# Optimization experiments

Measured on AMD Instinct MI355X. Metric: run time of the kernel, lower is better.

Reference implementation:

```python
import jax, jax.numpy as jnp
import numpy as np
from jax import lax

EPS_GN = 1e-5
EPS_LN = 1e-5
EPS_ADJ = 1e-6


def group_norm(x, g, b, groups=8, eps=EPS_GN):
    # x: (N, C, T); PyTorch GroupNorm: normalize over (C//groups, T) per group
    N, C, T = x.shape
    xr = x.reshape(N, groups, C // groups, T)
    m = xr.mean(axis=(2, 3), keepdims=True)
    v = xr.var(axis=(2, 3), keepdims=True)
    xr = (xr - m) * lax.rsqrt(v + eps)
    return xr.reshape(N, C, T) * g[None, :, None] + b[None, :, None]


def layer_norm(x, g, b, eps=EPS_LN):
    m = x.mean(axis=-1, keepdims=True)
    v = x.var(axis=-1, keepdims=True)
    return (x - m) * lax.rsqrt(v + eps) * g + b


def conv1d(x, w, stride, pad):
    # x: (N, Cin, T), w: (Cout, Cin, K), no bias
    return lax.conv_general_dilated(x, w, window_strides=(stride,), padding=[(pad, pad)],
                                    dimension_numbers=('NCH', 'OIH', 'NCH'))


def setup_inputs() -> dict:
    key = jax.random.key(0)
    ks = jax.random.split(key, 16)
    B, C, T = 256, 4, 4096
    TW, D, N = 64, 128, 4
    x = jax.random.normal(ks[0], (B, C, T), dtype=jnp.float32)
    conv1_w = jax.random.normal(ks[1], (TW, 1, 9), dtype=jnp.float32) * 0.1
    gn1_g = jnp.ones((TW,), jnp.float32)
    gn1_b = jnp.zeros((TW,), jnp.float32)
    conv2_w = jax.random.normal(ks[2], (TW, TW, 7), dtype=jnp.float32) * 0.05
    gn2_g = jnp.ones((TW,), jnp.float32)
    gn2_b = jnp.zeros((TW,), jnp.float32)
    proj_w = jax.random.normal(ks[3], (D, TW), dtype=jnp.float32) * 0.1
    proj_b = jnp.zeros((D,), jnp.float32)
    A = jnp.eye(N, dtype=jnp.float32) + 0.05 * jax.random.normal(ks[4], (N, N), dtype=jnp.float32)
    lin1_w = jax.random.normal(ks[5], (D, D), dtype=jnp.float32) * 0.08
    ln1_g = jnp.ones((D,), jnp.float32)
    ln1_b = jnp.zeros((D,), jnp.float32)
    lin2_w = jax.random.normal(ks[6], (D, D), dtype=jnp.float32) * 0.08
    ln2_g = jnp.ones((D,), jnp.float32)
    ln2_b = jnp.zeros((D,), jnp.float32)
    on_g = jnp.ones((D,), jnp.float32)
    on_b = jnp.zeros((D,), jnp.float32)
    return dict(x=x, conv1_w=conv1_w, gn1_g=gn1_g, gn1_b=gn1_b, conv2_w=conv2_w,
                gn2_g=gn2_g, gn2_b=gn2_b, proj_w=proj_w, proj_b=proj_b, A=A,
                lin1_w=lin1_w, ln1_g=ln1_g, ln1_b=ln1_b, lin2_w=lin2_w,
                ln2_g=ln2_g, ln2_b=ln2_b, on_g=on_g, on_b=on_b)


def reference(x, conv1_w, gn1_g, gn1_b, conv2_w, gn2_g, gn2_b, proj_w, proj_b, A,
              lin1_w, ln1_g, ln1_b, lin2_w, ln2_g, ln2_b, on_g, on_b):
    B, C, T = x.shape
    D = proj_w.shape[0]
    # The per-channel Python loop in the original shares the same temporal net;
    # fold channels into the batch dim and run the convs once.
    h = x.reshape(B * C, 1, T)
    h = jax.nn.gelu(group_norm(conv1d(h, conv1_w, 2, 4), gn1_g, gn1_b), approximate=False)
    h = jax.nn.gelu(group_norm(conv1d(h, conv2_w, 2, 3), gn2_g, gn2_b), approximate=False)
    h = h.mean(axis=-1)                      # (B*C, TW)
    v = h @ proj_w.T + proj_b                # (B*C, D)
    H = v.reshape(B, C, D)                   # node features, N = C channels
    # normalized adjacency: D^{-1/2} (A + I) D^{-1/2}
    A_tilde = A + jnp.eye(A.shape[0], dtype=A.dtype)
    deg = A_tilde.sum(axis=1)
    d_inv_sqrt = (deg + EPS_ADJ) ** -0.5
    A_hat = d_inv_sqrt[:, None] * A_tilde * d_inv_sqrt[None, :]
    for lw, lg, lb in ((lin1_w, ln1_g, ln1_b), (lin2_w, ln2_g, ln2_b)):
        Hm = jnp.einsum('nm,bmd->bnd', A_hat, H)
        H = jax.nn.gelu(layer_norm(Hm @ lw.T, lg, lb), approximate=False)
    H = layer_norm(H, on_g, on_b)
    return H.mean(axis=1)                    # (B, D)
```

## Files before the change

### kernel.cpp

```cpp
#include <hip/hip_runtime.h>
#include <hip/hip_fp16.h>
#include <math.h>

#define NS   1024
#define TIN  4096
#define T1   2048
#define T2   1024
#define TW   64
#define NG   8
#define DD   128

typedef __attribute__((ext_vector_type(8))) _Float16 f16x8;
typedef __attribute__((ext_vector_type(4))) float    f32x4;

__device__ __forceinline__ float gelu_fast(float x) {
  float t = x * x;
  float p = fmaf(0.044715f, t, 1.0f);
  float u = 2.3022038f * x * p;
  float e = exp2f(u);
  float r = __builtin_amdgcn_rcpf(e + 1.0f);
  return fmaf(-x, r, x);
}

__global__ __launch_bounds__(64) void k_stats1(
    const float* __restrict__ x, const float* __restrict__ w1,
    float* __restrict__ stats1) {
  int n = blockIdx.x;
  __shared__ float xw[4112];
  const float* xr = x + (size_t)n * TIN;
  for (int i = threadIdx.x; i < 4112; i += 64) {
    int xi = i - 4;
    xw[i] = (xi >= 0 && xi < TIN) ? xr[xi] : 0.f;
  }
  __syncthreads();
  float C[45], S[9];
#pragma unroll
  for (int c = 0; c < 45; c++) C[c] = 0.f;
#pragma unroll
  for (int i = 0; i < 9; i++) S[i] = 0.f;
  int l = threadIdx.x;
  for (int j = 0; j < 32; j++) {
    int t = l + 64 * j;
    float w[9];
#pragma unroll
    for (int i = 0; i < 9; i++) w[i] = xw[2 * t + i];
#pragma unroll
    for (int i = 0; i < 9; i++) S[i] += w[i];
    int c = 0;
#pragma unroll
    for (int i = 0; i < 9; i++)
#pragma unroll
      for (int jj = i; jj < 9; jj++) { C[c] = fmaf(w[i], w[jj], C[c]); c++; }
  }
#pragma unroll
  for (int off = 1; off < 64; off <<= 1) {
#pragma unroll
    for (int i = 0; i < 9; i++) S[i] += __shfl_xor(S[i], off, 64);
#pragma unroll
    for (int c = 0; c < 45; c++) C[c] += __shfl_xor(C[c], off, 64);
  }
  float wv[9];
#pragma unroll
  for (int i = 0; i < 9; i++) wv[i] = w1[l * 9 + i];
  float sm = 0.f, sq = 0.f;
  {
    int c = 0;
#pragma unroll
    for (int i = 0; i < 9; i++) {
      sm = fmaf(wv[i], S[i], sm);
#pragma unroll
      for (int jj = i; jj < 9; jj++) {
        float f = (jj == i) ? wv[i] * wv[jj] : 2.f * wv[i] * wv[jj];
        sq = fmaf(f, C[c], sq); c++;
      }
    }
  }
#pragma unroll
  for (int off = 1; off < 8; off <<= 1) {
    sm += __shfl_xor(sm, off, 64);
    sq += __shfl_xor(sq, off, 64);
  }
  if ((l & 7) == 0) {
    float m = sm * (1.f / 16384.f);
    float v = sq * (1.f / 16384.f) - m * m;
    stats1[(n * NG + (l >> 3)) * 2 + 0] = m;
    stats1[(n * NG + (l >> 3)) * 2 + 1] = rsqrtf(v + 1e-5f);
  }
}

__global__ __launch_bounds__(256) void k_prep(
    const float* __restrict__ w2, const float* __restrict__ w1,
    _Float16* __restrict__ w2tf, _Float16* __restrict__ w1h) {
  int idx = blockIdx.x * 256 + threadIdx.x;
  if (idx < 7 * 64 * 64) {
    int kk = idx >> 12;
    int r = idx & 4095;
    int co = r >> 6, ci = r & 63;
    w2tf[idx] = (_Float16)w2[(co * 64 + ci) * 7 + kk];
  } else {
    int r = idx - 28672;
    if (r < 64 * 32) {
      int ci = r >> 5, k = r & 31;
      w1h[r] = (k < 9) ? (_Float16)w1[ci * 9 + k] : (_Float16)0.f;
    }
  }
}

__global__ __launch_bounds__(256, 6) void k_conv(
    const float* __restrict__ x, const _Float16* __restrict__ w1h,
    const float* __restrict__ g1, const float* __restrict__ b1,
    const float* __restrict__ stats1, const _Float16* __restrict__ w2tf,
    __half* __restrict__ y2, float* __restrict__ stats2) {
  constexpr int ROWS = 144, HS = 72;
  __shared__ _Float16 h1s[ROWS * HS];
  __shared__ _Float16 xh[320];
  __shared__ float scs[TW], bss[TW];

  const int tid = threadIdx.x;
  const int n = blockIdx.x >> 4;
  const int tile = blockIdx.x & 15;
  const int t0 = tile << 6;
  const bool chk = (tile == 0) || (tile == 15);

  const float* xr = x + (size_t)n * TIN;
  for (int i = tid; i < 320; i += 256) {
    int xi = 4 * t0 - 10 + i;
    xh[i] = (i < 278 && xi >= 0 && xi < TIN) ? (_Float16)xr[xi] : (_Float16)0.f;
  }
  if (tid < TW) {
    int ci = tid, g = ci >> 3;
    float m = stats1[(n * NG + g) * 2 + 0];
    float is = stats1[(n * NG + g) * 2 + 1];
    float s = is * g1[ci];
    scs[ci] = s;
    bss[ci] = b1[ci] - m * s;
  }
  __syncthreads();

  const int lane = tid & 63;
  const int wv = tid >> 6;
  const int m = lane & 15;
  const int q = lane >> 4;

  {
    f16x8 w1f[4];
#pragma unroll
    for (int nt = 0; nt < 4; nt++)
      w1f[nt] = *(const f16x8*)&w1h[(nt * 16 + m) * 32 + 8 * q];
    float sc4[4], bs4[4];
#pragma unroll
    for (int nt = 0; nt < 4; nt++) {
      sc4[nt] = scs[nt * 16 + m];
      bs4[nt] = bss[nt * 16 + m];
    }
    for (int mt = wv; mt < 9; mt += 4) {
      int r0 = mt * 16;
      int xi0 = 2 * (r0 + m) + 8 * q;
      uint4 uu;
      uu.x = *(const unsigned*)&xh[xi0 + 0];
      uu.y = *(const unsigned*)&xh[xi0 + 2];
      uu.z = *(const unsigned*)&xh[xi0 + 4];
      uu.w = *(const unsigned*)&xh[xi0 + 6];
      f16x8 af = __builtin_bit_cast(f16x8, uu);
      int rowb = r0 + 4 * q;
#pragma unroll
      for (int nt = 0; nt < 4; nt++) {
        f32x4 d = __builtin_amdgcn_mfma_f32_16x16x32_f16(
            af, w1f[nt], (f32x4){0.f, 0.f, 0.f, 0.f}, 0, 0, 0);
#pragma unroll
        for (int r = 0; r < 4; r++) {
          float v = gelu_fast(fmaf(d[r], sc4[nt], bs4[nt]));
          if (chk) {
            int tp = 2 * t0 - 3 + rowb + r;
            if ((unsigned)tp >= (unsigned)T1) v = 0.f;
          }
          h1s[(rowb + r) * HS + nt * 16 + m] = (_Float16)v;
        }
      }
    }
  }
  __syncthreads();

  const int co0 = wv * 16 + m;
  f32x4 acc[4];
#pragma unroll
  for (int mt = 0; mt < 4; mt++) acc[mt] = (f32x4){0.f, 0.f, 0.f, 0.f};

  for (int kk = 0; kk < 7; kk++) {
    f16x8 bfr[2];
#pragma unroll
    for (int ks = 0; ks < 2; ks++)
      bfr[ks] = *(const f16x8*)&w2tf[(kk * 64 + co0) * 64 + 32 * ks + 8 * q];
#pragma unroll
    for (int mt = 0; mt < 4; mt++) {
      int tl = 2 * (mt * 16 + m) + kk;
      f16x8 a0 = *(const f16x8*)&h1s[tl * HS + 8 * q];
      f16x8 a1 = *(const f16x8*)&h1s[tl * HS + 32 + 8 * q];
      acc[mt] = __builtin_amdgcn_mfma_f32_16x16x32_f16(a0, bfr[0], acc[mt], 0, 0, 0);
      acc[mt] = __builtin_amdgcn_mfma_f32_16x16x32_f16(a1, bfr[1], acc[mt], 0, 0, 0);
    }
  }

  float sum = 0.f, ssq = 0.f;
#pragma unroll
  for (int mt = 0; mt < 4; mt++)
#pragma unroll
    for (int r = 0; r < 4; r++) {
      float v = acc[mt][r];
      sum += v; ssq += v * v;
    }
  sum += __shfl_xor(sum, 1, 64);  ssq += __shfl_xor(ssq, 1, 64);
  sum += __shfl_xor(sum, 2, 64);  ssq += __shfl_xor(ssq, 2, 64);
  sum += __shfl_xor(sum, 4, 64);  ssq += __shfl_xor(ssq, 4, 64);
  sum += __shfl_xor(sum, 16, 64); ssq += __shfl_xor(ssq, 16, 64);
  sum += __shfl_xor(sum, 32, 64); ssq += __shfl_xor(ssq, 32, 64);
  if (lane == 0 || lane == 8) {
    int g = 2 * wv + (lane >> 3);
    atomicAdd(&stats2[(n * NG + g) * 2 + 0], sum);
    atomicAdd(&stats2[(n * NG + g) * 2 + 1], ssq);
  }

  __syncthreads();
  __half* tr = (__half*)h1s;
#pragma unroll
  for (int mt = 0; mt < 4; mt++)
#pragma unroll
    for (int r = 0; r < 4; r++) {
      int t = mt * 16 + q * 4 + r;
      tr[t * HS + co0] = __float2half(acc[mt][r]);
    }
  __syncthreads();
  for (int idx = tid; idx < 512; idx += 256) {
    int t = idx >> 3, c8 = (idx & 7) * 8;
    float4 v = *(float4*)&tr[t * HS + c8];
    *(float4*)&y2[((size_t)(n * 1024) + t0 + t) * 64 + c8] = v;
  }
}

__global__ __launch_bounds__(256) void k_gn2mean(
    const __half* __restrict__ y2, const float* __restrict__ stats2,
    const float* __restrict__ g2, const float* __restrict__ b2,
    float* __restrict__ hbar) {
  int n = blockIdx.x;
  int coct = threadIdx.x & 7;
  int tsl = threadIdx.x >> 3;
  int co0 = coct * 8;
  float mn = stats2[(n * NG + coct) * 2 + 0] * (1.f / 8192.f);
  float e2 = stats2[(n * NG + coct) * 2 + 1] * (1.f / 8192.f);
  float istd = rsqrtf(e2 - mn * mn + 1e-5f);
  float sca[8], sh[8];
#pragma unroll
  for (int j = 0; j < 8; j++) {
    sca[j] = istd * g2[co0 + j];
    sh[j] = b2[co0 + j] - mn * sca[j];
  }
  const __half* base = y2 + (size_t)n * 65536;
  float a[8];
#pragma unroll
  for (int j = 0; j < 8; j++) a[j] = 0.f;
  for (int i = 0; i < 32; i++) {
    int t = tsl + 32 * i;
    float4 raw = *(const float4*)&base[t * 64 + co0];
    __half2 hh[4];
    *(float4*)hh = raw;
#pragma unroll
    for (int p = 0; p < 4; p++) {
      float2 f = __half22float2(hh[p]);
      a[2 * p]     += gelu_fast(fmaf(f.x, sca[2 * p], sh[2 * p]));
      a[2 * p + 1] += gelu_fast(fmaf(f.y, sca[2 * p + 1], sh[2 * p + 1]));
    }
  }
  __shared__ float red[32][64];
  *(float4*)&red[tsl][co0] = *(float4*)&a[0];
  *(float4*)&red[tsl][co0 + 4] = *(float4*)&a[4];
  __syncthreads();
  if (threadIdx.x < 64) {
    float s = 0.f;
#pragma unroll 8
    for (int r = 0; r < 32; r++) s += red[r][threadIdx.x];
    hbar[n * 64 + threadIdx.x] = s;
  }
}

__global__ __launch_bounds__(256) void k_head(
    const float* __restrict__ hbar,
    const float* __restrict__ pw, const float* __restrict__ pb,
    const float* __restrict__ A,
    const float* __restrict__ l1w, const float* __restrict__ l1g, const float* __restrict__ l1b,
    const float* __restrict__ l2w, const float* __restrict__ l2g, const float* __restrict__ l2b,
    const float* __restrict__ og, const float* __restrict__ ob,
    float* __restrict__ out) {
  int b = blockIdx.x;
  __shared__ float h4[4][TW];
  __shared__ float H[4][DD];
  __shared__ float Hm[4][DD];
  __shared__ float Xs[4][DD];
  __shared__ float At[16], Ah[16], dinv[4];
  {
    int i = threadIdx.x;
    int c = i >> 6, k = i & 63;
    h4[c][k] = hbar[(b * 4 + c) * TW + k] * (1.f / 1024.f);
  }
  if (threadIdx.x < 16)
    At[threadIdx.x] = A[threadIdx.x] + ((threadIdx.x % 5) == 0 ? 1.f : 0.f);
  __syncthreads();
  if (threadIdx.x < 4) {
    float dg = At[threadIdx.x * 4] + At[threadIdx.x * 4 + 1] +
               At[threadIdx.x * 4 + 2] + At[threadIdx.x * 4 + 3];
    dinv[threadIdx.x] = rsqrtf(dg + 1e-6f);
  }
  for (int idx = threadIdx.x; idx < 512; idx += 256) {
    int c = idx >> 7, d = idx & 127;
    float acc = pb[d];
    const float* wrow = pw + d * TW;
#pragma unroll 8
    for (int k = 0; k < TW; k++) acc += h4[c][k] * wrow[k];
    H[c][d] = acc;
  }
  __syncthreads();
  if (threadIdx.x < 16)
    Ah[threadIdx.x] = dinv[threadIdx.x >> 2] * At[threadIdx.x] * dinv[threadIdx.x & 3];
  __syncthreads();
  for (int L = 0; L < 2; L++) {
    const float* lw = L ? l2w : l1w;
    const float* lg = L ? l2g : l1g;
    const float* lb = L ? l2b : l1b;
    for (int idx = threadIdx.x; idx < 512; idx += 256) {
      int nn = idx >> 7, d = idx & 127;
      Hm[nn][d] = Ah[nn * 4 + 0] * H[0][d] + Ah[nn * 4 + 1] * H[1][d] +
                  Ah[nn * 4 + 2] * H[2][d] + Ah[nn * 4 + 3] * H[3][d];
    }
    __syncthreads();
    for (int idx = threadIdx.x; idx < 512; idx += 256) {
      int nn = idx >> 7, d = idx & 127;
      float acc = 0.f;
      const float* wrow = lw + d * DD;
#pragma unroll 8
      for (int k = 0; k < DD; k++) acc += Hm[nn][k] * wrow[k];
      Xs[nn][d] = acc;
    }
    __syncthreads();
    {
      int w = threadIdx.x >> 6, lane = threadIdx.x & 63;
      float v0 = Xs[w][lane], v1 = Xs[w][lane + 64];
      float s = v0 + v1, qq = v0 * v0 + v1 * v1;
#pragma unroll
      for (int off = 1; off < 64; off <<= 1) {
        s += __shfl_xor(s, off, 64);
        qq += __shfl_xor(qq, off, 64);
      }
      float mm = s * (1.f / 128.f);
      float istd = rsqrtf(qq * (1.f / 128.f) - mm * mm + 1e-5f);
      H[w][lane]      = gelu_fast((v0 - mm) * istd * lg[lane] + lb[lane]);
      H[w][lane + 64] = gelu_fast((v1 - mm) * istd * lg[lane + 64] + lb[lane + 64]);
    }
    __syncthreads();
  }
  {
    int w = threadIdx.x >> 6, lane = threadIdx.x & 63;
    float v0 = H[w][lane], v1 = H[w][lane + 64];
    float s = v0 + v1, qq = v0 * v0 + v1 * v1;
#pragma unroll
    for (int off = 1; off < 64; off <<= 1) {
      s += __shfl_xor(s, off, 64);
      qq += __shfl_xor(qq, off, 64);
    }
    float mm = s * (1.f / 128.f);
    float istd = rsqrtf(qq * (1.f / 128.f) - mm * mm + 1e-5f);
    Xs[w][lane]      = (v0 - mm) * istd * og[lane] + ob[lane];
    Xs[w][lane + 64] = (v1 - mm) * istd * og[lane + 64] + ob[lane + 64];
  }
  __syncthreads();
  if (threadIdx.x < DD) {
    int d = threadIdx.x;
    out[b * DD + d] = 0.25f * (Xs[0][d] + Xs[1][d] + Xs[2][d] + Xs[3][d]);
  }
}

extern "C" void kernel_launch(void* const* d_in, const int* in_sizes, int n_in,
                              void* d_out, int out_size, void* d_ws, size_t ws_size,
                              hipStream_t stream) {
  (void)in_sizes; (void)n_in; (void)out_size; (void)ws_size;
  const float* x       = (const float*)d_in[0];
  const float* conv1_w = (const float*)d_in[1];
  const float* gn1_g   = (const float*)d_in[2];
  const float* gn1_b   = (const float*)d_in[3];
  const float* conv2_w = (const float*)d_in[4];
  const float* gn2_g   = (const float*)d_in[5];
  const float* gn2_b   = (const float*)d_in[6];
  const float* proj_w  = (const float*)d_in[7];
  const float* proj_b  = (const float*)d_in[8];
  const float* A       = (const float*)d_in[9];
  const float* lin1_w  = (const float*)d_in[10];
  const float* ln1_g   = (const float*)d_in[11];
  const float* ln1_b   = (const float*)d_in[12];
  const float* lin2_w  = (const float*)d_in[13];
  const float* ln2_g   = (const float*)d_in[14];
  const float* ln2_b   = (const float*)d_in[15];
  const float* on_g    = (const float*)d_in[16];
  const float* on_b    = (const float*)d_in[17];
  float* out = (float*)d_out;

  float* wsf = (float*)d_ws;
  float* stats2 = wsf;
  float* stats1 = wsf + 16384;
  float* hbar   = wsf + 32768;
  _Float16* w2tf = (_Float16*)(wsf + 98304);
  _Float16* w1h  = (_Float16*)(wsf + 112640);
  __half* y2h    = (__half*)(wsf + 113664);

  hipMemsetAsync(stats2, 0, 16384 * sizeof(float), stream);
  k_prep<<<120, 256, 0, stream>>>(conv2_w, conv1_w, w2tf, w1h);
  k_stats1<<<NS, 64, 0, stream>>>(x, conv1_w, stats1);
  k_conv<<<NS * 16, 256, 0, stream>>>(x, w1h, gn1_g, gn1_b, stats1, w2tf,
                                      y2h, stats2);
  k_gn2mean<<<NS, 256, 0, stream>>>(y2h, stats2, gn2_g, gn2_b, hbar);
  k_head<<<256, 256, 0, stream>>>(hbar, proj_w, proj_b, A,
                                  lin1_w, ln1_g, ln1_b,
                                  lin2_w, ln2_g, ln2_b,
                                  on_g, on_b, out);
}
```

Measured before the change: 331.8 us.

## Fuse conv2, GN2 stats and GELU-mean into one per-sample block kernel

Replaces the tiled conv kernel plus separate GN2+mean kernel with a single 1024-thread block per sample that computes all 16 time tiles in four passes. Conv2 outputs stay in registers as packed fp16, group statistics are reduced in shared memory, and GELU+mean is applied directly. This removes the y2 global round-trip, the stats2 atomics and memset, and one launch. In exchange it needs 32 held registers per thread, a large LDS footprint (about 92KB), fewer blocks (1024), and more block-wide barriers, all of which may limit occupancy.

```diff
diff --git a/kernel.cpp b/kernel.cpp
--- a/kernel.cpp
+++ b/kernel.cpp
@@ -106,61 +106,72 @@
   }
 }
 
-__global__ __launch_bounds__(256, 6) void k_conv(
+__global__ __launch_bounds__(1024, 4) void k_fused(
     const float* __restrict__ x, const _Float16* __restrict__ w1h,
     const float* __restrict__ g1, const float* __restrict__ b1,
     const float* __restrict__ stats1, const _Float16* __restrict__ w2tf,
-    __half* __restrict__ y2, float* __restrict__ stats2) {
-  constexpr int ROWS = 144, HS = 72;
-  __shared__ _Float16 h1s[ROWS * HS];
-  __shared__ _Float16 xh[320];
+    const float* __restrict__ g2, const float* __restrict__ b2,
+    float* __restrict__ hbar) {
+  constexpr int HS = 72;
+  __shared__ _Float16 xh[4160];
+  __shared__ _Float16 h1s[4][144 * HS];
   __shared__ float scs[TW], bss[TW];
+  __shared__ float redS[256], redQ[256];
+  __shared__ float scb[TW], shb[TW];
 
   const int tid = threadIdx.x;
-  const int n = blockIdx.x >> 4;
-  const int tile = blockIdx.x & 15;
-  const int t0 = tile << 6;
-  const bool chk = (tile == 0) || (tile == 15);
-
+  const int n = blockIdx.x;
   const float* xr = x + (size_t)n * TIN;
-  for (int i = tid; i < 320; i += 256) {
-    int xi = 4 * t0 - 10 + i;
-    xh[i] = (i < 278 && xi >= 0 && xi < TIN) ? (_Float16)xr[xi] : (_Float16)0.f;
+  for (int i = tid; i < 4160; i += 1024) {
+    int xi = i - 10;
+    xh[i] = (xi >= 0 && xi < TIN) ? (_Float16)xr[xi] : (_Float16)0.f;
   }
   if (tid < TW) {
     int ci = tid, g = ci >> 3;
-    float m = stats1[(n * NG + g) * 2 + 0];
+    float mn = stats1[(n * NG + g) * 2 + 0];
     float is = stats1[(n * NG + g) * 2 + 1];
     float s = is * g1[ci];
     scs[ci] = s;
-    bss[ci] = b1[ci] - m * s;
-  }
-  __syncthreads();
-
+    bss[ci] = b1[ci] - mn * s;
+  }
+  __syncthreads();
+
+  const int w = tid >> 6;
   const int lane = tid & 63;
-  const int wv = tid >> 6;
   const int m = lane & 15;
   const int q = lane >> 4;
-
-  {
-    f16x8 w1f[4];
-#pragma unroll
-    for (int nt = 0; nt < 4; nt++)
-      w1f[nt] = *(const f16x8*)&w1h[(nt * 16 + m) * 32 + 8 * q];
-    float sc4[4], bs4[4];
-#pragma unroll
-    for (int nt = 0; nt < 4; nt++) {
-      sc4[nt] = scs[nt * 16 + m];
-      bs4[nt] = bss[nt * 16 + m];
-    }
-    for (int mt = wv; mt < 9; mt += 4) {
+  const int ti = w >> 2;
+  const int wvt = w & 3;
+  const int co0 = wvt * 16 + m;
+
+  f16x8 w1f[4];
+#pragma unroll
+  for (int nt = 0; nt < 4; nt++)
+    w1f[nt] = *(const f16x8*)&w1h[(nt * 16 + m) * 32 + 8 * q];
+  float sc4[4], bs4[4];
+#pragma unroll
+  for (int nt = 0; nt < 4; nt++) {
+    sc4[nt] = scs[nt * 16 + m];
+    bs4[nt] = bss[nt * 16 + m];
+  }
+
+  unsigned held[32];
+  float ssum = 0.f, ssq = 0.f;
+
+  for (int it = 0; it < 4; it++) {
+    const int tg = it * 4 + ti;
+    const int t0 = tg << 6;
+    const bool chk = (tg == 0) || (tg == 15);
+    __syncthreads();
+
+    for (int mt = wvt; mt < 9; mt += 4) {
       int r0 = mt * 16;
-      int xi0 = 2 * (r0 + m) + 8 * q;
+      int xg = 4 * t0 + 2 * (r0 + m) + 8 * q;
       uint4 uu;
-      uu.x = *(const unsigned*)&xh[xi0 + 0];
-      uu.y = *(const unsigned*)&xh[xi0 + 2];
-      uu.z = *(const unsigned*)&xh[xi0 + 4];
-      uu.w = *(const unsigned*)&xh[xi0 + 6];
+      uu.x = *(const unsigned*)&xh[xg + 0];
+      uu.y = *(const unsigned*)&xh[xg + 2];
+      uu.z = *(const unsigned*)&xh[xg + 4];
+      uu.w = *(const unsigned*)&xh[xg + 6];
       f16x8 af = __builtin_bit_cast(f16x8, uu);
       int rowb = r0 + 4 * q;
 #pragma unroll
@@ -174,111 +185,80 @@
             int tp = 2 * t0 - 3 + rowb + r;
             if ((unsigned)tp >= (unsigned)T1) v = 0.f;
           }
-          h1s[(rowb + r) * HS + nt * 16 + m] = (_Float16)v;
+          h1s[ti][(rowb + r) * HS + nt * 16 + m] = (_Float16)v;
         }
       }
     }
-  }
-  __syncthreads();
-
-  const int co0 = wv * 16 + m;
-  f32x4 acc[4];
-#pragma unroll
-  for (int mt = 0; mt < 4; mt++) acc[mt] = (f32x4){0.f, 0.f, 0.f, 0.f};
-
-  for (int kk = 0; kk < 7; kk++) {
-    f16x8 bfr[2];
-#pragma unroll
-    for (int ks = 0; ks < 2; ks++)
-      bfr[ks] = *(const f16x8*)&w2tf[(kk * 64 + co0) * 64 + 32 * ks + 8 * q];
-#pragma unroll
-    for (int mt = 0; mt < 4; mt++) {
-      int tl = 2 * (mt * 16 + m) + kk;
-      f16x8 a0 = *(const f16x8*)&h1s[tl * HS + 8 * q];
-      f16x8 a1 = *(const f16x8*)&h1s[tl * HS + 32 + 8 * q];
-      acc[mt] = __builtin_amdgcn_mfma_f32_16x16x32_f16(a0, bfr[0], acc[mt], 0, 0, 0);
-      acc[mt] = __builtin_amdgcn_mfma_f32_16x16x32_f16(a1, bfr[1], acc[mt], 0, 0, 0);
-    }
-  }
-
-  float sum = 0.f, ssq = 0.f;
-#pragma unroll
-  for (int mt = 0; mt < 4; mt++)
-#pragma unroll
-    for (int r = 0; r < 4; r++) {
-      float v = acc[mt][r];
-      sum += v; ssq += v * v;
-    }
-  sum += __shfl_xor(sum, 1, 64);  ssq += __shfl_xor(ssq, 1, 64);
-  sum += __shfl_xor(sum, 2, 64);  ssq += __shfl_xor(ssq, 2, 64);
-  sum += __shfl_xor(sum, 4, 64);  ssq += __shfl_xor(ssq, 4, 64);
-  sum += __shfl_xor(sum, 16, 64); ssq += __shfl_xor(ssq, 16, 64);
-  sum += __shfl_xor(sum, 32, 64); ssq += __shfl_xor(ssq, 32, 64);
-  if (lane == 0 || lane == 8) {
-    int g = 2 * wv + (lane >> 3);
-    atomicAdd(&stats2[(n * NG + g) * 2 + 0], sum);
-    atomicAdd(&stats2[(n * NG + g) * 2 + 1], ssq);
-  }
-
-  __syncthreads();
-  __half* tr = (__half*)h1s;
-#pragma unroll
-  for (int mt = 0; mt < 4; mt++)
-#pragma unroll
-    for (int r = 0; r < 4; r++) {
-      int t = mt * 16 + q * 4 + r;
-      tr[t * HS + co0] = __float2half(acc[mt][r]);
-    }
-  __syncthreads();
-  for (int idx = tid; idx < 512; idx += 256) {
-    int t = idx >> 3, c8 = (idx & 7) * 8;
-    float4 v = *(float4*)&tr[t * HS + c8];
-    *(float4*)&y2[((size_t)(n * 1024) + t0 + t) * 64 + c8] = v;
-  }
-}
-
-__global__ __launch_bounds__(256) void k_gn2mean(
-    const __half* __restrict__ y2, const float* __restrict__ stats2,
-    const float* __restrict__ g2, const float* __restrict__ b2,
-    float* __restrict__ hbar) {
-  int n = blockIdx.x;
-  int coct = threadIdx.x & 7;
-  int tsl = threadIdx.x >> 3;
-  int co0 = coct * 8;
-  float mn = stats2[(n * NG + coct) * 2 + 0] * (1.f / 8192.f);
-  float e2 = stats2[(n * NG + coct) * 2 + 1] * (1.f / 8192.f);
-  float istd = rsqrtf(e2 - mn * mn + 1e-5f);
-  float sca[8], sh[8];
-#pragma unroll
-  for (int j = 0; j < 8; j++) {
-    sca[j] = istd * g2[co0 + j];
-    sh[j] = b2[co0 + j] - mn * sca[j];
-  }
-  const __half* base = y2 + (size_t)n * 65536;
-  float a[8];
-#pragma unroll
-  for (int j = 0; j < 8; j++) a[j] = 0.f;
+    __syncthreads();
+
+    f32x4 acc[4];
+#pragma unroll
+    for (int mt = 0; mt < 4; mt++) acc[mt] = (f32x4){0.f, 0.f, 0.f, 0.f};
+    for (int kk = 0; kk < 7; kk++) {
+      f16x8 bf0 = *(const f16x8*)&w2tf[(kk * 64 + co0) * 64 + 8 * q];
+      f16x8 bf1 = *(const f16x8*)&w2tf[(kk * 64 + co0) * 64 + 32 + 8 * q];
+#pragma unroll
+      for (int mt = 0; mt < 4; mt++) {
+        int tl = 2 * (mt * 16 + m) + kk;
+        f16x8 a0 = *(const f16x8*)&h1s[ti][tl * HS + 8 * q];
+        f16x8 a1 = *(const f16x8*)&h1s[ti][tl * HS + 32 + 8 * q];
+        acc[mt] = __builtin_amdgcn_mfma_f32_16x16x32_f16(a0, bf0, acc[mt], 0, 0, 0);
+        acc[mt] = __builtin_amdgcn_mfma_f32_16x16x32_f16(a1, bf1, acc[mt], 0, 0, 0);
+      }
+    }
+
+#pragma unroll
+    for (int mt = 0; mt < 4; mt++)
+#pragma unroll
+      for (int pr = 0; pr < 2; pr++) {
+        float lo = acc[mt][2 * pr], hi = acc[mt][2 * pr + 1];
+        ssum += lo + hi;
+        ssq += lo * lo + hi * hi;
+        held[it * 8 + mt * 2 + pr] =
+            __builtin_bit_cast(unsigned, __builtin_amdgcn_cvt_pkrtz(lo, hi));
+      }
+  }
+
+  ssum += __shfl_xor(ssum, 16, 64); ssq += __shfl_xor(ssq, 16, 64);
+  ssum += __shfl_xor(ssum, 32, 64); ssq += __shfl_xor(ssq, 32, 64);
+  if (q == 0) { redS[w * 16 + m] = ssum; redQ[w * 16 + m] = ssq; }
+  __syncthreads();
+  if (tid < 64) {
+    int wt = tid >> 4, mm = tid & 15;
+    float s  = redS[wt * 16 + mm] + redS[(wt + 4) * 16 + mm] +
+               redS[(wt + 8) * 16 + mm] + redS[(wt + 12) * 16 + mm];
+    float q2 = redQ[wt * 16 + mm] + redQ[(wt + 4) * 16 + mm] +
+               redQ[(wt + 8) * 16 + mm] + redQ[(wt + 12) * 16 + mm];
+    s  += __shfl_xor(s, 1, 64);  q2 += __shfl_xor(q2, 1, 64);
+    s  += __shfl_xor(s, 2, 64);  q2 += __shfl_xor(q2, 2, 64);
+    s  += __shfl_xor(s, 4, 64);  q2 += __shfl_xor(q2, 4, 64);
+    float mn = s * (1.f / 8192.f);
+    float e2 = q2 * (1.f / 8192.f);
+    float istd = rsqrtf(e2 - mn * mn + 1e-5f);
+    float sca = istd * g2[tid];
+    scb[tid] = sca;
+    shb[tid] = b2[tid] - mn * sca;
+  }
+  __syncthreads();
+
+  float sca = scb[co0], sh = shb[co0];
+  float tsum = 0.f;
+#pragma unroll
   for (int i = 0; i < 32; i++) {
-    int t = tsl + 32 * i;
-    float4 raw = *(const float4*)&base[t * 64 + co0];
-    __half2 hh[4];
-    *(float4*)hh = raw;
-#pragma unroll
-    for (int p = 0; p < 4; p++) {
-      float2 f = __half22float2(hh[p]);
-      a[2 * p]     += gelu_fast(fmaf(f.x, sca[2 * p], sh[2 * p]));
-      a[2 * p + 1] += gelu_fast(fmaf(f.y, sca[2 * p + 1], sh[2 * p + 1]));
-    }
-  }
-  __shared__ float red[32][64];
-  *(float4*)&red[tsl][co0] = *(float4*)&a[0];
-  *(float4*)&red[tsl][co0 + 4] = *(float4*)&a[4];
-  __syncthreads();
-  if (threadIdx.x < 64) {
-    float s = 0.f;
-#pragma unroll 8
-    for (int r = 0; r < 32; r++) s += red[r][threadIdx.x];
-    hbar[n * 64 + threadIdx.x] = s;
+    __half2 hh = __builtin_bit_cast(__half2, held[i]);
+    float2 f = __half22float2(hh);
+    tsum += gelu_fast(fmaf(f.x, sca, sh)) + gelu_fast(fmaf(f.y, sca, sh));
+  }
+  tsum += __shfl_xor(tsum, 16, 64);
+  tsum += __shfl_xor(tsum, 32, 64);
+  __syncthreads();
+  if (q == 0) redS[w * 16 + m] = tsum;
+  __syncthreads();
+  if (tid < 64) {
+    int wt = tid >> 4, mm = tid & 15;
+    float s = redS[wt * 16 + mm] + redS[(wt + 4) * 16 + mm] +
+              redS[(wt + 8) * 16 + mm] + redS[(wt + 12) * 16 + mm];
+    hbar[n * TW + tid] = s;
   }
 }
 
@@ -402,19 +382,15 @@
   float* out = (float*)d_out;
 
   float* wsf = (float*)d_ws;
-  float* stats2 = wsf;
-  float* stats1 = wsf + 16384;
-  float* hbar   = wsf + 32768;
-  _Float16* w2tf = (_Float16*)(wsf + 98304);
-  _Float16* w1h  = (_Float16*)(wsf + 112640);
-  __half* y2h    = (__half*)(wsf + 113664);
-
-  hipMemsetAsync(stats2, 0, 16384 * sizeof(float), stream);
+  float* stats1 = wsf;
+  float* hbar   = wsf + 16384;
+  _Float16* w2tf = (_Float16*)(wsf + 81920);
+  _Float16* w1h  = w2tf + 28672;
+
   k_prep<<<120, 256, 0, stream>>>(conv2_w, conv1_w, w2tf, w1h);
   k_stats1<<<NS, 64, 0, stream>>>(x, conv1_w, stats1);
-  k_conv<<<NS * 16, 256, 0, stream>>>(x, w1h, gn1_g, gn1_b, stats1, w2tf,
-                                      y2h, stats2);
-  k_gn2mean<<<NS, 256, 0, stream>>>(y2h, stats2, gn2_g, gn2_b, hbar);
+  k_fused<<<NS, 1024, 0, stream>>>(x, w1h, gn1_g, gn1_b, stats1, w2tf,
+                                   gn2_g, gn2_b, hbar);
   k_head<<<256, 256, 0, stream>>>(hbar, proj_w, proj_b, A,
                                   lin1_w, ln1_g, ln1_b,
                                   lin2_w, ln2_g, ln2_b,
```

Result: slower. 416.1 us (+25.4%).

## Transpose conv1 MFMA output, pad LDS rows, and reorder conv2 weights per output channel

Applied to the files above, without the earlier changes.

The conv1 MFMA operands are swapped so each lane holds four consecutive channels of one row. The four GELU outputs are then packed to fp16 and written to LDS as a single 8-byte store, replacing four scalar stores, and the boundary mask is evaluated once per row. The LDS row stride changes from 72 to 76 halves to alter the bank pattern. The conv2 weights are re-laid out as [co][kk][ci] and the kk loop is fully unrolled with precomputed pointers. Occupancy bounds drop from 6 to 4 blocks per CU, and the fp16 conversion switches to round-toward-zero.

```diff
diff --git a/kernel.cpp b/kernel.cpp
--- a/kernel.cpp
+++ b/kernel.cpp
@@ -93,9 +93,9 @@
     _Float16* __restrict__ w2tf, _Float16* __restrict__ w1h) {
   int idx = blockIdx.x * 256 + threadIdx.x;
   if (idx < 7 * 64 * 64) {
-    int kk = idx >> 12;
-    int r = idx & 4095;
-    int co = r >> 6, ci = r & 63;
+    int co = idx / 448;
+    int r = idx % 448;
+    int kk = r >> 6, ci = r & 63;
     w2tf[idx] = (_Float16)w2[(co * 64 + ci) * 7 + kk];
   } else {
     int r = idx - 28672;
@@ -106,15 +106,15 @@
   }
 }
 
-__global__ __launch_bounds__(256, 6) void k_conv(
+#define HS 76
+__global__ __launch_bounds__(256, 4) void k_conv(
     const float* __restrict__ x, const _Float16* __restrict__ w1h,
     const float* __restrict__ g1, const float* __restrict__ b1,
     const float* __restrict__ stats1, const _Float16* __restrict__ w2tf,
     __half* __restrict__ y2, float* __restrict__ stats2) {
-  constexpr int ROWS = 144, HS = 72;
-  __shared__ _Float16 h1s[ROWS * HS];
+  __shared__ _Float16 h1s[144 * HS];
   __shared__ _Float16 xh[320];
-  __shared__ float scs[TW], bss[TW];
+  __shared__ __align__(16) float scs[TW], bss[TW];
 
   const int tid = threadIdx.x;
   const int n = blockIdx.x >> 4;
@@ -147,35 +147,39 @@
 #pragma unroll
     for (int nt = 0; nt < 4; nt++)
       w1f[nt] = *(const f16x8*)&w1h[(nt * 16 + m) * 32 + 8 * q];
-    float sc4[4], bs4[4];
+    float4 scv[4], bsv[4];
 #pragma unroll
     for (int nt = 0; nt < 4; nt++) {
-      sc4[nt] = scs[nt * 16 + m];
-      bs4[nt] = bss[nt * 16 + m];
+      scv[nt] = *(const float4*)&scs[nt * 16 + 4 * q];
+      bsv[nt] = *(const float4*)&bss[nt * 16 + 4 * q];
     }
     for (int mt = wv; mt < 9; mt += 4) {
-      int r0 = mt * 16;
-      int xi0 = 2 * (r0 + m) + 8 * q;
+      int row = mt * 16 + m;
+      int xg = 2 * row + 8 * q;
       uint4 uu;
-      uu.x = *(const unsigned*)&xh[xi0 + 0];
-      uu.y = *(const unsigned*)&xh[xi0 + 2];
-      uu.z = *(const unsigned*)&xh[xi0 + 4];
-      uu.w = *(const unsigned*)&xh[xi0 + 6];
-      f16x8 af = __builtin_bit_cast(f16x8, uu);
-      int rowb = r0 + 4 * q;
+      uu.x = *(const unsigned*)&xh[xg + 0];
+      uu.y = *(const unsigned*)&xh[xg + 2];
+      uu.z = *(const unsigned*)&xh[xg + 4];
+      uu.w = *(const unsigned*)&xh[xg + 6];
+      f16x8 bf = __builtin_bit_cast(f16x8, uu);
+      bool oor = false;
+      if (chk) {
+        int tp = 2 * t0 - 3 + row;
+        oor = ((unsigned)tp >= (unsigned)T1);
+      }
 #pragma unroll
       for (int nt = 0; nt < 4; nt++) {
         f32x4 d = __builtin_amdgcn_mfma_f32_16x16x32_f16(
-            af, w1f[nt], (f32x4){0.f, 0.f, 0.f, 0.f}, 0, 0, 0);
-#pragma unroll
-        for (int r = 0; r < 4; r++) {
-          float v = gelu_fast(fmaf(d[r], sc4[nt], bs4[nt]));
-          if (chk) {
-            int tp = 2 * t0 - 3 + rowb + r;
-            if ((unsigned)tp >= (unsigned)T1) v = 0.f;
-          }
-          h1s[(rowb + r) * HS + nt * 16 + m] = (_Float16)v;
-        }
+            w1f[nt], bf, (f32x4){0.f, 0.f, 0.f, 0.f}, 0, 0, 0);
+        float v0 = gelu_fast(fmaf(d[0], scv[nt].x, bsv[nt].x));
+        float v1 = gelu_fast(fmaf(d[1], scv[nt].y, bsv[nt].y));
+        float v2 = gelu_fast(fmaf(d[2], scv[nt].z, bsv[nt].z));
+        float v3 = gelu_fast(fmaf(d[3], scv[nt].w, bsv[nt].w));
+        uint2 pk;
+        pk.x = __builtin_bit_cast(unsigned, __builtin_amdgcn_cvt_pkrtz(v0, v1));
+        pk.y = __builtin_bit_cast(unsigned, __builtin_amdgcn_cvt_pkrtz(v2, v3));
+        if (oor) { pk.x = 0u; pk.y = 0u; }
+        *(uint2*)&h1s[row * HS + nt * 16 + 4 * q] = pk;
       }
     }
   }
@@ -186,19 +190,33 @@
 #pragma unroll
   for (int mt = 0; mt < 4; mt++) acc[mt] = (f32x4){0.f, 0.f, 0.f, 0.f};
 
+  const _Float16* wp = w2tf + co0 * 448 + 8 * q;
+  const _Float16* ap0 = &h1s[(2 * (0 * 16 + m)) * HS + 8 * q];
+  const _Float16* ap1 = &h1s[(2 * (1 * 16 + m)) * HS + 8 * q];
+  const _Float16* ap2 = &h1s[(2 * (2 * 16 + m)) * HS + 8 * q];
+  const _Float16* ap3 = &h1s[(3 * 16 + m) * 2 * HS + 8 * q];
+
+#pragma unroll
   for (int kk = 0; kk < 7; kk++) {
-    f16x8 bfr[2];
-#pragma unroll
-    for (int ks = 0; ks < 2; ks++)
-      bfr[ks] = *(const f16x8*)&w2tf[(kk * 64 + co0) * 64 + 32 * ks + 8 * q];
-#pragma unroll
-    for (int mt = 0; mt < 4; mt++) {
-      int tl = 2 * (mt * 16 + m) + kk;
-      f16x8 a0 = *(const f16x8*)&h1s[tl * HS + 8 * q];
-      f16x8 a1 = *(const f16x8*)&h1s[tl * HS + 32 + 8 * q];
-      acc[mt] = __builtin_amdgcn_mfma_f32_16x16x32_f16(a0, bfr[0], acc[mt], 0, 0, 0);
-      acc[mt] = __builtin_amdgcn_mfma_f32_16x16x32_f16(a1, bfr[1], acc[mt], 0, 0, 0);
-    }
+    f16x8 b0 = *(const f16x8*)(wp + kk * 64);
+    f16x8 b1 = *(const f16x8*)(wp + kk * 64 + 32);
+    f16x8 a;
+    a = *(const f16x8*)(ap0 + kk * HS);
+    acc[0] = __builtin_amdgcn_mfma_f32_16x16x32_f16(a, b0, acc[0], 0, 0, 0);
+    a = *(const f16x8*)(ap0 + kk * HS + 32);
+    acc[0] = __builtin_amdgcn_mfma_f32_16x16x32_f16(a, b1, acc[0], 0, 0, 0);
+    a = *(const f16x8*)(ap1 + kk * HS);
+    acc[1] = __builtin_amdgcn_mfma_f32_16x16x32_f16(a, b0, acc[1], 0, 0, 0);
+    a = *(const f16x8*)(ap1 + kk * HS + 32);
+    acc[1] = __builtin_amdgcn_mfma_f32_16x16x32_f16(a, b1, acc[1], 0, 0, 0);
+    a = *(const f16x8*)(ap2 + kk * HS);
+    acc[2] = __builtin_amdgcn_mfma_f32_16x16x32_f16(a, b0, acc[2], 0, 0, 0);
+    a = *(const f16x8*)(ap2 + kk * HS + 32);
+    acc[2] = __builtin_amdgcn_mfma_f32_16x16x32_f16(a, b1, acc[2], 0, 0, 0);
+    a = *(const f16x8*)(ap3 + kk * HS);
+    acc[3] = __builtin_amdgcn_mfma_f32_16x16x32_f16(a, b0, acc[3], 0, 0, 0);
+    a = *(const f16x8*)(ap3 + kk * HS + 32);
+    acc[3] = __builtin_amdgcn_mfma_f32_16x16x32_f16(a, b1, acc[3], 0, 0, 0);
   }
 
   float sum = 0.f, ssq = 0.f;
```

Result: slower. 421.0 us (+26.9%).
